# Kernel tuning notes

Measured on AMD Instinct MI355X. Metric: run time of the kernel, lower is better.

Reference implementation:

```python
import jax, jax.numpy as jnp
import numpy as np

B, DIM, N = 4, 256, 2048
HEADS, DIM_HEAD = 8, 64
HIDDEN = HEADS * DIM_HEAD
SCALE = DIM_HEAD ** -0.5


def setup_inputs() -> dict:
    key = jax.random.key(0)
    k0, k1, k2, k3 = jax.random.split(key, 4)
    x = jax.random.normal(k0, (B, DIM, N), dtype=jnp.float32)
    # Conv1d kernel-size-1 weights == plain matrices over channels
    w_qkv = jax.random.normal(k1, (3 * HIDDEN, DIM), dtype=jnp.float32) * (DIM ** -0.5)
    w_out = jax.random.normal(k2, (DIM, HIDDEN), dtype=jnp.float32) * (HIDDEN ** -0.5)
    b_out = jax.random.normal(k3, (DIM,), dtype=jnp.float32) * 0.01
    return {"x": x, "w_qkv": w_qkv, "w_out": w_out, "b_out": b_out}


def reference(x, w_qkv, w_out, b_out):
    b, c, n = x.shape
    # 1x1 conv projection: [3H, C] x [b, C, n] -> [b, 3H, n]
    qkv = jnp.einsum('oc,bcn->bon', w_qkv, x)
    q, k, v = jnp.split(qkv, 3, axis=1)
    # [b, heads, dim_head, n]
    q = q.reshape(b, HEADS, DIM_HEAD, n) * SCALE
    k = k.reshape(b, HEADS, DIM_HEAD, n)
    v = v.reshape(b, HEADS, DIM_HEAD, n)
    sim = jnp.einsum('bhcn,bhcm->bhnm', q, k)          # [b,h,n,n]
    attn = jax.nn.softmax(sim, axis=-1)
    out = jnp.einsum('bhnm,bhcm->bhcn', attn, v)       # [b,h,dh,n]
    out = out.reshape(b, HIDDEN, n)
    return jnp.einsum('oc,bcn->bon', w_out, out) + b_out[None, :, None]
```

## Files before the change

### kernel.cpp

```cpp
#include <hip/hip_runtime.h>
#include <math.h>

#define BB 4
#define CDIM 256
#define NN 2048
#define HEADS 8
#define DH 64
#define HIDDEN 512
#define THREEH 1536
#define QSCALE 0.18033688011112042f

typedef __attribute__((ext_vector_type(8))) short bf16x8;
typedef __attribute__((ext_vector_type(4))) float f32x4;
typedef __attribute__((ext_vector_type(4))) unsigned uint4v;

static __device__ inline unsigned short f2bf(float f) {
    unsigned u = __float_as_uint(f);
    u += 0x7fff + ((u >> 16) & 1);
    return (unsigned short)(u >> 16);
}
#if __has_builtin(__builtin_amdgcn_cvt_pk_bf16_f32)
static __device__ inline unsigned pk2(float a, float b) {
    auto v = __builtin_amdgcn_cvt_pk_bf16_f32(a, b);
    return __builtin_bit_cast(unsigned, v);
}
#else
static __device__ inline unsigned pk2(float a, float b) {
    return (unsigned)f2bf(a) | ((unsigned)f2bf(b) << 16);
}
#endif
#if __has_builtin(__builtin_amdgcn_exp2f)
#define EXP2(x) __builtin_amdgcn_exp2f(x)
#else
#define EXP2(x) exp2f(x)
#endif
#define MFMA16(a, b, c) __builtin_amdgcn_mfma_f32_16x16x32_bf16(a, b, c, 0, 0, 0)
#define SWZC(row, ch) ((((ch) ^ ((row) & 7)) << 3))

static __device__ inline void swap16(unsigned &a, unsigned &b) {
    asm("v_permlane16_swap_b32 %0, %1" : "+v"(a), "+v"(b));
}
static __device__ inline void swap32(unsigned &a, unsigned &b) {
    asm("v_permlane32_swap_b32 %0, %1" : "+v"(a), "+v"(b));
}

__global__ __launch_bounds__(256) void prep_all(const float* __restrict__ x,
                                                const float* __restrict__ wqkv,
                                                const float* __restrict__ wout,
                                                unsigned short* __restrict__ Xt,
                                                unsigned* __restrict__ Wqb,
                                                unsigned* __restrict__ Wob) {
    __shared__ float Ls[64][65];
    const int bx = blockIdx.x;
    if (bx < 512) {
        const int n0 = (bx & 31) * 64, c0 = ((bx >> 5) & 3) * 64, b = bx >> 7;
        const int t = threadIdx.x;
        const int r16 = t >> 4, c16 = t & 15;
#pragma unroll
        for (int s = 0; s < 4; ++s) {
            const int c = s * 16 + r16;
            float4 v = *(const float4*)&x[((size_t)(b * CDIM + c0 + c)) * NN + n0 + c16 * 4];
            *(float4*)&Ls[c][c16 * 4] = v;
        }
        __syncthreads();
#pragma unroll
        for (int s = 0; s < 4; ++s) {
            const int n = s * 16 + r16;
            const int c4 = c16 * 4;
            uint2 u;
            u.x = pk2(Ls[c4][n], Ls[c4 + 1][n]);
            u.y = pk2(Ls[c4 + 2][n], Ls[c4 + 3][n]);
            *(uint2*)&Xt[((size_t)(b * NN) + n0 + n) * CDIM + c0 + c4] = u;
        }
    } else if (bx < 536) {
        const int tt = (bx - 512) * 256 + threadIdx.x;
#pragma unroll 4
        for (int j = 0; j < 16; ++j) {
            const int i4 = tt + j * 6144;
            const int e = i4 * 4;
            const float s = ((e >> 8) < HIDDEN) ? QSCALE : 1.f;
            float4 v = *(const float4*)&wqkv[e];
            Wqb[i4 * 2 + 0] = pk2(v.x * s, v.y * s);
            Wqb[i4 * 2 + 1] = pk2(v.z * s, v.w * s);
        }
    } else {
        const int tt = (bx - 536) * 256 + threadIdx.x;
#pragma unroll 4
        for (int j = 0; j < 16; ++j) {
            const int i4 = tt + j * 2048;
            const int e = i4 * 4;
            float4 v = *(const float4*)&wout[e];
            Wob[i4 * 2 + 0] = pk2(v.x, v.y);
            Wob[i4 * 2 + 1] = pk2(v.z, v.w);
        }
    }
}

__global__ __launch_bounds__(256, 3) void qkv_gemm(const unsigned short* __restrict__ Xt,
                                                   const unsigned short* __restrict__ Wqb,
                                                   unsigned short* __restrict__ Qb,
                                                   unsigned short* __restrict__ Kb,
                                                   unsigned short* __restrict__ Vb) {
    __shared__ unsigned short Xs[128 * 64], Ws[128 * 64];
    const int bn0 = blockIdx.x * 128, o0 = blockIdx.y * 128;
    const int t = threadIdx.x, l = t & 63, w = t >> 6, lo = l & 15, quad = l >> 4;
    const int wo = (w >> 1) * 64, wn = (w & 1) * 64;
    const int sr = t >> 1, scb = (t & 1) * 4;
    const bool isV = (o0 >= 2 * HIDDEN);
    f32x4 acc[4][4];
#pragma unroll
    for (int i = 0; i < 4; ++i)
#pragma unroll
        for (int j = 0; j < 4; ++j) acc[i][j] = (f32x4){0.f, 0.f, 0.f, 0.f};

    for (int kc = 0; kc < CDIM; kc += 64) {
        __syncthreads();
#pragma unroll
        for (int j = 0; j < 4; ++j) {
            const int ch = scb + j;
            *(uint4*)&Xs[sr * 64 + SWZC(sr, ch)] =
                *(const uint4*)&Xt[(size_t)(bn0 + sr) * CDIM + kc + ch * 8];
            *(uint4*)&Ws[sr * 64 + SWZC(sr, ch)] =
                *(const uint4*)&Wqb[(size_t)(o0 + sr) * CDIM + kc + ch * 8];
        }
        __syncthreads();
#pragma unroll
        for (int kk = 0; kk < 2; ++kk) {
            const int swz = SWZC(lo, kk * 4 + quad);
            if (!isV) {
                bf16x8 af[4], bv[4];
#pragma unroll
                for (int ot = 0; ot < 4; ++ot) af[ot] = *(const bf16x8*)&Ws[(wo + ot * 16 + lo) * 64 + swz];
#pragma unroll
                for (int nt = 0; nt < 4; ++nt) bv[nt] = *(const bf16x8*)&Xs[(wn + nt * 16 + lo) * 64 + swz];
#pragma unroll
                for (int ot = 0; ot < 4; ++ot)
#pragma unroll
                    for (int nt = 0; nt < 4; ++nt) acc[ot][nt] = MFMA16(af[ot], bv[nt], acc[ot][nt]);
            } else {
                bf16x8 af[4], bv[4];
#pragma unroll
                for (int mt = 0; mt < 4; ++mt) af[mt] = *(const bf16x8*)&Xs[(wn + mt * 16 + lo) * 64 + swz];
#pragma unroll
                for (int ot = 0; ot < 4; ++ot) bv[ot] = *(const bf16x8*)&Ws[(wo + ot * 16 + lo) * 64 + swz];
#pragma unroll
                for (int mt = 0; mt < 4; ++mt)
#pragma unroll
                    for (int ot = 0; ot < 4; ++ot) acc[mt][ot] = MFMA16(af[mt], bv[ot], acc[mt][ot]);
            }
        }
    }
    if (!isV) {
#pragma unroll
        for (int ot = 0; ot < 4; ++ot) {
            const int og = o0 + wo + ot * 16 + quad * 4;
            const int h = (og >> 6) & 7;
            const int c0 = og & 63;
            unsigned short* dst = (og >= HIDDEN) ? Kb : Qb;
#pragma unroll
            for (int nt = 0; nt < 4; ++nt) {
                const int bn = bn0 + wn + nt * 16 + lo;
                const int b = bn >> 11, n = bn & 2047;
                uint2 u;
                u.x = pk2(acc[ot][nt][0], acc[ot][nt][1]);
                u.y = pk2(acc[ot][nt][2], acc[ot][nt][3]);
                *(uint2*)&dst[(((size_t)(b * HEADS + h)) * NN + n) * DH + c0] = u;
            }
        }
    } else {
#pragma unroll
        for (int mt = 0; mt < 4; ++mt) {
            const int bn = bn0 + wn + mt * 16 + quad * 4;
            const int b = bn >> 11, m = bn & 2047;
#pragma unroll
            for (int ot = 0; ot < 4; ++ot) {
                const int og = o0 + wo + ot * 16 + lo;
                const int h = (og >> 6) & 7;
                const int c = og & 63;
                uint2 u;
                u.x = pk2(acc[mt][ot][0], acc[mt][ot][1]);
                u.y = pk2(acc[mt][ot][2], acc[mt][ot][3]);
                *(uint2*)&Vb[(((size_t)(b * HEADS + h)) * DH + c) * NN + m] = u;
            }
        }
    }
}

__global__ __launch_bounds__(256, 4) void flash_attn(const unsigned short* __restrict__ Qb,
                                                     const unsigned short* __restrict__ Kb,
                                                     const unsigned short* __restrict__ Vb,
                                                     float* __restrict__ Op,
                                                     float* __restrict__ lp) {
    __shared__ unsigned short Ks[64 * 64], Vs[64 * 64];
    const int flat = blockIdx.x;
    const int sp = flat >> 9;
    const int f2 = flat & 511;
    const int rest = f2 >> 3;
    const int bh = ((rest & 3) << 3) | (f2 & 7);
    const int q0 = (rest >> 2) * 128;
    const int t = threadIdx.x, l = t & 63, w = t >> 6, lo = l & 15, quad = l >> 4;
    const unsigned short* Qp = Qb + (size_t)bh * NN * DH;
    const unsigned short* Kp = Kb + (size_t)bh * NN * DH;
    const unsigned short* Vp = Vb + (size_t)bh * DH * NN;
    const int kv0 = sp * (NN / 2), kvEnd = kv0 + NN / 2;
    const int qbase = q0 + 32 * w;
    bf16x8 bQ[2][2];
#pragma unroll
    for (int qt = 0; qt < 2; ++qt)
#pragma unroll
        for (int hh = 0; hh < 2; ++hh)
            bQ[qt][hh] = *(const bf16x8*)&Qp[(size_t)(qbase + qt * 16 + lo) * DH + hh * 32 + quad * 8];
    f32x4 O[4][2], lacc[2];
#pragma unroll
    for (int i = 0; i < 4; ++i)
#pragma unroll
        for (int j = 0; j < 2; ++j) O[i][j] = (f32x4){0.f, 0.f, 0.f, 0.f};
#pragma unroll
    for (int j = 0; j < 2; ++j) lacc[j] = (f32x4){0.f, 0.f, 0.f, 0.f};
    const int sr = t >> 3, sc = t & 7;
    const int kst0 = sr * 64 + SWZC(sr, sc);
    bf16x8 aOnes;
    {
        const short v = (lo == 0) ? (short)0x3F80 : (short)0;
        aOnes = (bf16x8){v, v, v, v, v, v, v, v};
    }
    uint4 rk0 = *(const uint4*)&Kp[(size_t)(kv0 + sr) * DH + sc * 8];
    uint4 rk1 = *(const uint4*)&Kp[(size_t)(kv0 + sr + 32) * DH + sc * 8];
    uint4 rv0 = *(const uint4*)&Vp[(size_t)sr * NN + kv0 + sc * 8];
    uint4 rv1 = *(const uint4*)&Vp[(size_t)(sr + 32) * NN + kv0 + sc * 8];

#pragma unroll 1
    for (int m0 = kv0; m0 < kvEnd; m0 += 64) {
        __syncthreads();
        *(uint4*)&Ks[kst0] = rk0;
        *(uint4*)&Ks[kst0 + 2048] = rk1;
        *(uint4*)&Vs[kst0] = rv0;
        *(uint4*)&Vs[kst0 + 2048] = rv1;
        __syncthreads();
        {
            const int m1 = (m0 + 64 < kvEnd) ? (m0 + 64) : m0;
            rk0 = *(const uint4*)&Kp[(size_t)(m1 + sr) * DH + sc * 8];
            rk1 = *(const uint4*)&Kp[(size_t)(m1 + sr + 32) * DH + sc * 8];
            rv0 = *(const uint4*)&Vp[(size_t)sr * NN + m1 + sc * 8];
            rv1 = *(const uint4*)&Vp[(size_t)(sr + 32) * NN + m1 + sc * 8];
        }
        unsigned wv[2][4][2];
#pragma unroll
        for (int nt = 0; nt < 4; ++nt) {
            const int rb = (nt * 16 + lo) * 64;
            bf16x8 a0 = *(const bf16x8*)&Ks[rb + SWZC(lo, quad)];
            bf16x8 a1 = *(const bf16x8*)&Ks[rb + SWZC(lo, quad + 4)];
#pragma unroll
            for (int qt = 0; qt < 2; ++qt) {
                f32x4 z = (f32x4){0.f, 0.f, 0.f, 0.f};
                z = MFMA16(a0, bQ[qt][0], z);
                z = MFMA16(a1, bQ[qt][1], z);
                wv[qt][nt][0] = pk2(EXP2(z[0]), EXP2(z[1]));
                wv[qt][nt][1] = pk2(EXP2(z[2]), EXP2(z[3]));
            }
        }
        bf16x8 pb[2][2];
#pragma unroll
        for (int qt = 0; qt < 2; ++qt) {
#pragma unroll
            for (int f = 0; f < 2; ++f) {
                unsigned x0 = wv[qt][2 * f][0], y0 = wv[qt][2 * f + 1][0];
                unsigned x1 = wv[qt][2 * f][1], y1 = wv[qt][2 * f + 1][1];
                swap32(x0, y0); swap16(x0, y0);
                swap32(x1, y1); swap16(x1, y1);
                uint4v uu;
                uu.x = x0; uu.y = x1; uu.z = y0; uu.w = y1;
                pb[qt][f] = __builtin_bit_cast(bf16x8, uu);
            }
        }
#pragma unroll
        for (int ct = 0; ct < 4; ++ct) {
            const int rb = (ct * 16 + lo) * 64;
            bf16x8 a0 = *(const bf16x8*)&Vs[rb + SWZC(lo, quad)];
            bf16x8 a1 = *(const bf16x8*)&Vs[rb + SWZC(lo, quad + 4)];
#pragma unroll
            for (int qt = 0; qt < 2; ++qt) {
                O[ct][qt] = MFMA16(a0, pb[qt][0], O[ct][qt]);
                O[ct][qt] = MFMA16(a1, pb[qt][1], O[ct][qt]);
            }
        }
#pragma unroll
        for (int qt = 0; qt < 2; ++qt) {
            lacc[qt] = MFMA16(aOnes, pb[qt][0], lacc[qt]);
            lacc[qt] = MFMA16(aOnes, pb[qt][1], lacc[qt]);
        }
    }
#pragma unroll
    for (int qt = 0; qt < 2; ++qt) {
        const int q = qbase + qt * 16 + lo;
        float* orow = Op + ((size_t)(sp * 32 + bh) * NN + q) * DH;
#pragma unroll
        for (int ct = 0; ct < 4; ++ct) {
            *(f32x4*)&orow[ct * 16 + quad * 4] = O[ct][qt];
        }
        if (quad == 0) lp[(size_t)(sp * 32 + bh) * NN + q] = lacc[qt][0];
    }
}

__global__ __launch_bounds__(256) void combine(const float* __restrict__ Op,
                                               const float* __restrict__ lp,
                                               unsigned short* __restrict__ Yb) {
    const int t = blockIdx.x * 256 + threadIdx.x;
    const int c4 = (t & 15) * 4;
    const int q = (t >> 4) & (NN - 1);
    const int bh = t >> 15;
    const size_t half = (size_t)32 * NN * DH;
    const size_t base = ((size_t)bh * NN + q) * DH + c4;
    f32x4 o0 = *(const f32x4*)&Op[base];
    f32x4 o1 = *(const f32x4*)&Op[base + half];
    const float inv = 1.f / (lp[(size_t)bh * NN + q] + lp[(size_t)32 * NN + (size_t)bh * NN + q]);
    uint2 u;
    u.x = pk2((o0[0] + o1[0]) * inv, (o0[1] + o1[1]) * inv);
    u.y = pk2((o0[2] + o1[2]) * inv, (o0[3] + o1[3]) * inv);
    const int b = bh >> 3, h = bh & 7;
    *(uint2*)&Yb[((size_t)(b * NN + q)) * HIDDEN + h * DH + c4] = u;
}

__global__ __launch_bounds__(256, 4) void out_gemm(const unsigned short* __restrict__ Yb,
                                                   const unsigned short* __restrict__ Wob,
                                                   const float* __restrict__ bias,
                                                   float* __restrict__ out) {
    __shared__ unsigned short Ys[128 * 64], Wos[64 * 64];
    const int bn0 = blockIdx.x * 128, o0 = blockIdx.y * 64;
    const int t = threadIdx.x, l = t & 63, w = t >> 6, lo = l & 15, quad = l >> 4;
    const int wn = w * 32;
    const int sr = t >> 1, scb = (t & 1) * 4;
    const int sr2 = t >> 2, scb2 = (t & 3) * 2;
    f32x4 acc[2][4];
#pragma unroll
    for (int i = 0; i < 2; ++i)
#pragma unroll
        for (int j = 0; j < 4; ++j) acc[i][j] = (f32x4){0.f, 0.f, 0.f, 0.f};

    for (int kc = 0; kc < HIDDEN; kc += 64) {
        __syncthreads();
#pragma unroll
        for (int j = 0; j < 4; ++j) {
            const int ch = scb + j;
            *(uint4*)&Ys[sr * 64 + SWZC(sr, ch)] =
                *(const uint4*)&Yb[(size_t)(bn0 + sr) * HIDDEN + kc + ch * 8];
        }
#pragma unroll
        for (int j = 0; j < 2; ++j) {
            const int ch = scb2 + j;
            *(uint4*)&Wos[sr2 * 64 + SWZC(sr2, ch)] =
                *(const uint4*)&Wob[(size_t)(o0 + sr2) * HIDDEN + kc + ch * 8];
        }
        __syncthreads();
#pragma unroll
        for (int kk = 0; kk < 2; ++kk) {
            const int swz = SWZC(lo, kk * 4 + quad);
            bf16x8 bv[4];
#pragma unroll
            for (int ot = 0; ot < 4; ++ot) bv[ot] = *(const bf16x8*)&Wos[(ot * 16 + lo) * 64 + swz];
#pragma unroll
            for (int mt = 0; mt < 2; ++mt) {
                bf16x8 av = *(const bf16x8*)&Ys[(wn + mt * 16 + lo) * 64 + swz];
#pragma unroll
                for (int ot = 0; ot < 4; ++ot) acc[mt][ot] = MFMA16(av, bv[ot], acc[mt][ot]);
            }
        }
    }
#pragma unroll
    for (int mt = 0; mt < 2; ++mt) {
        const int bn = bn0 + wn + mt * 16 + quad * 4;
        const int b = bn >> 11, n = bn & 2047;
#pragma unroll
        for (int ot = 0; ot < 4; ++ot) {
            const int o = o0 + ot * 16 + lo;
            *(f32x4*)&out[((size_t)(b * CDIM + o)) * NN + n] = acc[mt][ot] + bias[o];
        }
    }
}

extern "C" void kernel_launch(void* const* d_in, const int* in_sizes, int n_in,
                              void* d_out, int out_size, void* d_ws, size_t ws_size,
                              hipStream_t stream) {
    const float* x     = (const float*)d_in[0];
    const float* w_qkv = (const float*)d_in[1];
    const float* w_out = (const float*)d_in[2];
    const float* b_out = (const float*)d_in[3];
    float* out = (float*)d_out;

    unsigned short* Wqb = (unsigned short*)d_ws;
    unsigned short* Wob = Wqb + (size_t)THREEH * CDIM;
    unsigned short* Xt  = Wob + (size_t)CDIM * HIDDEN;
    unsigned short* Qb  = Xt + (size_t)BB * NN * CDIM;
    unsigned short* Kb  = Qb + (size_t)BB * HEADS * NN * DH;
    unsigned short* Vb  = Kb + (size_t)BB * HEADS * NN * DH;
    unsigned short* Yb  = Vb + (size_t)BB * HEADS * DH * NN;
    float* Op = (float*)(Yb + (size_t)BB * NN * HIDDEN);
    float* lp = Op + (size_t)2 * BB * HEADS * NN * DH;

    prep_all<<<544, 256, 0, stream>>>(x, w_qkv, w_out, Xt, (unsigned*)Wqb, (unsigned*)Wob);
    qkv_gemm<<<dim3(BB * NN / 128, THREEH / 128), 256, 0, stream>>>(Xt, Wqb, Qb, Kb, Vb);
    flash_attn<<<1024, 256, 0, stream>>>(Qb, Kb, Vb, Op, lp);
    combine<<<(BB * HEADS * NN * 16) / 256, 256, 0, stream>>>(Op, lp, Yb);
    out_gemm<<<dim3(BB * NN / 128, CDIM / 64), 256, 0, stream>>>(Yb, Wob, b_out, out);
}
```

Baseline: 150.7 us.

## Load K/V MFMA fragments directly from global memory, drop LDS staging

The flash attention kernel no longer stages K and V tiles through shared memory with two block barriers per iteration. Each wave now loads its MFMA operand fragments directly from global memory, relying on L1/L2 to serve the reuse across the four waves. It also wraps the MFMA groups in s_setprio to favour matrix issue. Removing the barriers and LDS traffic comes at the cost of four times the global/L1 traffic and less latency hiding, since the register prefetch of the next tile is gone.

Result: slower. 222.5 us (+47.6%).

```diff
diff --git a/kernel.cpp b/kernel.cpp
--- a/kernel.cpp
+++ b/kernel.cpp
@@ -191,7 +191,6 @@
                                                      const unsigned short* __restrict__ Vb,
                                                      float* __restrict__ Op,
                                                      float* __restrict__ lp) {
-    __shared__ unsigned short Ks[64 * 64], Vs[64 * 64];
     const int flat = blockIdx.x;
     const int sp = flat >> 9;
     const int f2 = flat & 511;
@@ -217,44 +216,32 @@
         for (int j = 0; j < 2; ++j) O[i][j] = (f32x4){0.f, 0.f, 0.f, 0.f};
 #pragma unroll
     for (int j = 0; j < 2; ++j) lacc[j] = (f32x4){0.f, 0.f, 0.f, 0.f};
-    const int sr = t >> 3, sc = t & 7;
-    const int kst0 = sr * 64 + SWZC(sr, sc);
     bf16x8 aOnes;
     {
         const short v = (lo == 0) ? (short)0x3F80 : (short)0;
         aOnes = (bf16x8){v, v, v, v, v, v, v, v};
     }
-    uint4 rk0 = *(const uint4*)&Kp[(size_t)(kv0 + sr) * DH + sc * 8];
-    uint4 rk1 = *(const uint4*)&Kp[(size_t)(kv0 + sr + 32) * DH + sc * 8];
-    uint4 rv0 = *(const uint4*)&Vp[(size_t)sr * NN + kv0 + sc * 8];
-    uint4 rv1 = *(const uint4*)&Vp[(size_t)(sr + 32) * NN + kv0 + sc * 8];
+    const unsigned short* kRow = Kp + (size_t)lo * DH + quad * 8;
+    const unsigned short* vRow = Vp + (size_t)lo * NN + quad * 8;
 
 #pragma unroll 1
     for (int m0 = kv0; m0 < kvEnd; m0 += 64) {
-        __syncthreads();
-        *(uint4*)&Ks[kst0] = rk0;
-        *(uint4*)&Ks[kst0 + 2048] = rk1;
-        *(uint4*)&Vs[kst0] = rv0;
-        *(uint4*)&Vs[kst0 + 2048] = rv1;
-        __syncthreads();
-        {
-            const int m1 = (m0 + 64 < kvEnd) ? (m0 + 64) : m0;
-            rk0 = *(const uint4*)&Kp[(size_t)(m1 + sr) * DH + sc * 8];
-            rk1 = *(const uint4*)&Kp[(size_t)(m1 + sr + 32) * DH + sc * 8];
-            rv0 = *(const uint4*)&Vp[(size_t)sr * NN + m1 + sc * 8];
-            rv1 = *(const uint4*)&Vp[(size_t)(sr + 32) * NN + m1 + sc * 8];
+        bf16x8 ka0[4], ka1[4];
+#pragma unroll
+        for (int nt = 0; nt < 4; ++nt) {
+            ka0[nt] = *(const bf16x8*)&kRow[(size_t)(m0 + nt * 16) * DH];
+            ka1[nt] = *(const bf16x8*)&kRow[(size_t)(m0 + nt * 16) * DH + 32];
         }
         unsigned wv[2][4][2];
 #pragma unroll
         for (int nt = 0; nt < 4; ++nt) {
-            const int rb = (nt * 16 + lo) * 64;
-            bf16x8 a0 = *(const bf16x8*)&Ks[rb + SWZC(lo, quad)];
-            bf16x8 a1 = *(const bf16x8*)&Ks[rb + SWZC(lo, quad + 4)];
 #pragma unroll
             for (int qt = 0; qt < 2; ++qt) {
                 f32x4 z = (f32x4){0.f, 0.f, 0.f, 0.f};
-                z = MFMA16(a0, bQ[qt][0], z);
-                z = MFMA16(a1, bQ[qt][1], z);
+                __builtin_amdgcn_s_setprio(1);
+                z = MFMA16(ka0[nt], bQ[qt][0], z);
+                z = MFMA16(ka1[nt], bQ[qt][1], z);
+                __builtin_amdgcn_s_setprio(0);
                 wv[qt][nt][0] = pk2(EXP2(z[0]), EXP2(z[1]));
                 wv[qt][nt][1] = pk2(EXP2(z[2]), EXP2(z[3]));
             }
@@ -275,14 +262,15 @@
         }
 #pragma unroll
         for (int ct = 0; ct < 4; ++ct) {
-            const int rb = (ct * 16 + lo) * 64;
-            bf16x8 a0 = *(const bf16x8*)&Vs[rb + SWZC(lo, quad)];
-            bf16x8 a1 = *(const bf16x8*)&Vs[rb + SWZC(lo, quad + 4)];
+            bf16x8 a0 = *(const bf16x8*)&vRow[(size_t)(ct * 16) * NN + m0];
+            bf16x8 a1 = *(const bf16x8*)&vRow[(size_t)(ct * 16) * NN + m0 + 32];
+            __builtin_amdgcn_s_setprio(1);
 #pragma unroll
             for (int qt = 0; qt < 2; ++qt) {
                 O[ct][qt] = MFMA16(a0, pb[qt][0], O[ct][qt]);
                 O[ct][qt] = MFMA16(a1, pb[qt][1], O[ct][qt]);
             }
+            __builtin_amdgcn_s_setprio(0);
         }
 #pragma unroll
         for (int qt = 0; qt < 2; ++qt) {
```
